# Kernel tuning notes

Hardware: AMD Instinct MI355X
Metric: run time of the kernel (lower is better)

## Reference

```python
import jax, jax.numpy as jnp
import numpy as np

HIDDEN = 512
EMBED = 50
VOCAB = 83


def setup_inputs() -> dict:
    key = jax.random.key(0)
    ks = jax.random.split(key, 20)
    T, B = 600, 256
    s = lambda n: 1.0 / np.sqrt(n)
    inp = {
        "in_char": jax.random.normal(ks[0], (B, VOCAB), jnp.float32),
        "hidden": jax.random.normal(ks[1], (1, B, HIDDEN), jnp.float32),
        "encoder_output": jax.random.normal(ks[2], (T, B, HIDDEN), jnp.float32),
        # attention params
        "W_hp": jax.random.uniform(ks[3], (HIDDEN, HIDDEN), jnp.float32, -s(HIDDEN), s(HIDDEN)),
        "b_hp": jnp.zeros((HIDDEN,), jnp.float32),
        "W_ep": jax.random.uniform(ks[4], (HIDDEN, HIDDEN), jnp.float32, -s(HIDDEN), s(HIDDEN)),
        "b_ep": jnp.zeros((HIDDEN,), jnp.float32),
        "w_v": jax.random.uniform(ks[5], (HIDDEN, 1), jnp.float32, -s(HIDDEN), s(HIDDEN)),
        "b_v": jnp.zeros((1,), jnp.float32),
        # context shrink
        "W_cs": jax.random.uniform(ks[6], (HIDDEN, EMBED * 5), jnp.float32, -s(HIDDEN), s(HIDDEN)),
        "b_cs": jnp.zeros((EMBED * 5,), jnp.float32),
        # embedding
        "emb": jax.random.normal(ks[7], (VOCAB, EMBED), jnp.float32),
        # GRU: input size = 6*EMBED = 300, hidden = 512; gates [r,z,n]
        "W_ih": jax.random.uniform(ks[8], (6 * EMBED, 3 * HIDDEN), jnp.float32, -s(HIDDEN), s(HIDDEN)),
        "b_ih": jnp.zeros((3 * HIDDEN,), jnp.float32),
        "W_hh": jax.random.uniform(ks[9], (HIDDEN, 3 * HIDDEN), jnp.float32, -s(HIDDEN), s(HIDDEN)),
        "b_hh": jnp.zeros((3 * HIDDEN,), jnp.float32),
        # classifier
        "W_out": jax.random.uniform(ks[10], (HIDDEN, VOCAB), jnp.float32, -s(HIDDEN), s(HIDDEN)),
        "b_out": jnp.zeros((VOCAB,), jnp.float32),
    }
    return inp


def reference(in_char, hidden, encoder_output, W_hp, b_hp, W_ep, b_ep, w_v, b_v,
              W_cs, b_cs, emb, W_ih, b_ih, W_hh, b_hh, W_out, b_out):
    # encoder_output: [T, B, H]; hidden: [1, B, H]
    enc_bt = jnp.transpose(encoder_output, (1, 0, 2))  # [B, T, H]
    # Bahdanau additive attention score
    hidden_attn = hidden @ W_hp + b_hp            # [1, B, H]
    hidden_attn = jnp.transpose(hidden_attn, (1, 0, 2))  # [B, 1, H]
    enc_attn = enc_bt @ W_ep + b_ep               # [B, T, H]
    res = jnp.tanh(enc_attn + hidden_attn)        # [B, T, H]
    scores = (res @ w_v + b_v)[..., 0]            # [B, T]
    attn_weights = jax.nn.softmax(scores, axis=1)  # [B, T]
    # context = enc^T @ attn: [B, H]
    context = jnp.einsum('bth,bt->bh', enc_bt, attn_weights)
    context = context @ W_cs + b_cs               # [B, 5*EMBED]
    # embedding of argmax char
    top1 = jnp.argmax(in_char, axis=1)            # [B]
    embed_char = emb[top1]                        # [B, EMBED]
    in_dec = jnp.concatenate([embed_char, context], axis=1)  # [B, 6*EMBED]
    # single GRU step (PyTorch gate order: r, z, n)
    h = hidden[0]                                 # [B, H]
    gi = in_dec @ W_ih + b_ih                     # [B, 3H]
    gh = h @ W_hh + b_hh                          # [B, 3H]
    H = h.shape[1]
    i_r, i_z, i_n = gi[:, :H], gi[:, H:2 * H], gi[:, 2 * H:]
    h_r, h_z, h_n = gh[:, :H], gh[:, H:2 * H], gh[:, 2 * H:]
    r = jax.nn.sigmoid(i_r + h_r)
    z = jax.nn.sigmoid(i_z + h_z)
    n = jnp.tanh(i_n + r * h_n)
    new_h = (1.0 - z) * n + z * h                 # [B, H]
    output = jax.nn.softmax(new_h @ W_out + b_out, axis=1)  # [B, VOCAB]
    return output, new_h[None], attn_weights
```

## Files before the change

### kernel.cpp

```cpp
#include <hip/hip_runtime.h>

typedef unsigned short u16;
typedef unsigned int   u32;
typedef __attribute__((ext_vector_type(8))) short s8v;
typedef __attribute__((ext_vector_type(4))) float f4v;

#define OUT1_OFF 21248
#define OUT2_OFF 152320

__device__ __forceinline__ float b2f(u16 u) { return __uint_as_float(((u32)u) << 16); }
__device__ __forceinline__ u16 f2b(float f) {
  u32 x = __float_as_uint(f);
  x += 0x7fffu + ((x >> 16) & 1u);
  return (u16)(x >> 16);
}
__device__ __forceinline__ float ldf(const void* p, int i, int f32) {
  return f32 ? ((const float*)p)[i] : b2f(((const u16*)p)[i]);
}
__device__ __forceinline__ void stf(void* p, int i, float v, int f32) {
  if (f32) ((float*)p)[i] = v;
  else     ((u16*)p)[i] = f2b(v);
}
__device__ __forceinline__ float tanh_fast(float x) {
  float e = __expf(2.f * x);
  return 1.f - 2.f * __builtin_amdgcn_rcpf(e + 1.f);
}
__device__ __forceinline__ float sigmoid_fast(float x) {
  return __builtin_amdgcn_rcpf(1.f + __expf(-x));
}

__global__ __launch_bounds__(64) void k_detect(const u32* __restrict__ hid, int* __restrict__ flag) {
  int lane = threadIdx.x;
  int cnt = 0;
#pragma unroll
  for (int i = 0; i < 8; i++) {
    u32 w = hid[lane * 8 + i];
    u32 e = (w >> 7) & 0xFF;
    cnt += (e >= 100 && e <= 135) ? 1 : 0;
  }
#pragma unroll
  for (int o = 32; o > 0; o >>= 1) cnt += __shfl_xor(cnt, o);
  if (lane == 0) *flag = (cnt < 400) ? 1 : 0;
}

__global__ __launch_bounds__(256) void k_transpose(const void* __restrict__ in, u16* __restrict__ out,
                                                   const int* __restrict__ flagp) {
  const int f32 = *flagp;
  __shared__ u16 tile[32][33];
  const int bx = blockIdx.x * 32;
  const int by = blockIdx.y * 32;
  const int tx = threadIdx.x, ty = threadIdx.y;
#pragma unroll
  for (int i = 0; i < 4; i++)
    tile[ty + i * 8][tx] = f2b(ldf(in, (by + ty + i * 8) * 512 + bx + tx, f32));
  __syncthreads();
#pragma unroll
  for (int i = 0; i < 4; i++)
    out[(bx + ty + i * 8) * 512 + by + tx] = tile[tx][ty + i * 8];
}

__global__ __launch_bounds__(256) void k_hidden_attn(const void* __restrict__ hidden,
                                                     const void* __restrict__ W_hp,
                                                     const void* __restrict__ b_hp,
                                                     const void* __restrict__ b_ep,
                                                     float* __restrict__ ha2,
                                                     const int* __restrict__ flagp) {
  const int f32 = *flagp;
  const int b0 = blockIdx.x * 8, tid = threadIdx.x;
  __shared__ __align__(16) float hh[512 * 8];
  for (int idx = tid; idx < 4096; idx += 256) {
    int k = idx >> 3, j = idx & 7;
    hh[idx] = ldf(hidden, (b0 + j) * 512 + k, f32);
  }
  __syncthreads();
  const int n0 = tid, n1 = tid + 256;
  float acc0[8], acc1[8];
#pragma unroll
  for (int j = 0; j < 8; j++) { acc0[j] = 0.f; acc1[j] = 0.f; }
  for (int k = 0; k < 512; k++) {
    float w0 = ldf(W_hp, k * 512 + n0, f32);
    float w1 = ldf(W_hp, k * 512 + n1, f32);
    const f4v* hp = (const f4v*)&hh[k * 8];
    f4v ha = hp[0], hb = hp[1];
#pragma unroll
    for (int j = 0; j < 4; j++) {
      acc0[j] += ha[j] * w0; acc1[j] += ha[j] * w1;
      acc0[j + 4] += hb[j] * w0; acc1[j + 4] += hb[j] * w1;
    }
  }
  const float bb0 = ldf(b_hp, n0, f32) + ldf(b_ep, n0, f32);
  const float bb1 = ldf(b_hp, n1, f32) + ldf(b_ep, n1, f32);
#pragma unroll
  for (int j = 0; j < 8; j++) {
    ha2[(b0 + j) * 512 + n0] = acc0[j] + bb0;
    ha2[(b0 + j) * 512 + n1] = acc1[j] + bb1;
  }
}

__global__ __launch_bounds__(256) void k_scores(const void* __restrict__ enc,
                                                const u16* __restrict__ Wt,
                                                const float* __restrict__ ha2,
                                                const void* __restrict__ w_v,
                                                float* __restrict__ partial,
                                                const int* __restrict__ flagp) {
  const int f32 = *flagp;
  __shared__ __align__(16) short As[128 * 64];
  __shared__ __align__(16) short Bs[128 * 64];
  const int tid = threadIdx.x;
  const int ntile = blockIdx.x;
  const int mtile = blockIdx.y;
  const int lane = tid & 63, wave = tid >> 6;
  const int wm = wave >> 1, wn = wave & 1;
  const int lane15 = lane & 15, quad = lane >> 4;

  const u16*   Ab = (const u16*)enc + (size_t)mtile * 128 * 512;
  const float* Af = (const float*)enc + (size_t)mtile * 128 * 512;
  const u16*   Bbase = Wt + (size_t)ntile * 128 * 512;

  int srow[4], sslot[4], skc[4];
#pragma unroll
  for (int c = 0; c < 4; c++) {
    int chunk = c * 256 + tid;
    srow[c] = chunk >> 3;
    sslot[c] = chunk & 7;
    skc[c] = sslot[c] ^ (srow[c] & 7);
  }

  int arow[4], brow[4];
#pragma unroll
  for (int i = 0; i < 4; i++) {
    arow[i] = wm * 64 + i * 16 + lane15;
    brow[i] = wn * 64 + i * 16 + lane15;
  }

  f4v acc[4][4];
#pragma unroll
  for (int i = 0; i < 4; i++)
#pragma unroll
    for (int j = 0; j < 4; j++) acc[i][j] = (f4v){0.f, 0.f, 0.f, 0.f};

  for (int k0 = 0; k0 < 512; k0 += 64) {
    s8v ga[4], gb[4];
    if (f32) {
#pragma unroll
      for (int c = 0; c < 4; c++) {
        const float* s = Af + k0 + srow[c] * 512 + skc[c] * 8;
        f4v lo = *(const f4v*)s, hi = *(const f4v*)(s + 4);
        s8v t;
#pragma unroll
        for (int j = 0; j < 4; j++) { t[j] = (short)f2b(lo[j]); t[j + 4] = (short)f2b(hi[j]); }
        ga[c] = t;
      }
    } else {
#pragma unroll
      for (int c = 0; c < 4; c++) ga[c] = *(const s8v*)(Ab + k0 + srow[c] * 512 + skc[c] * 8);
    }
#pragma unroll
    for (int c = 0; c < 4; c++) gb[c] = *(const s8v*)(Bbase + k0 + srow[c] * 512 + skc[c] * 8);
#pragma unroll
    for (int c = 0; c < 4; c++) *(s8v*)&As[srow[c] * 64 + sslot[c] * 8] = ga[c];
#pragma unroll
    for (int c = 0; c < 4; c++) *(s8v*)&Bs[srow[c] * 64 + sslot[c] * 8] = gb[c];
    __syncthreads();
#pragma unroll
    for (int kk2 = 0; kk2 < 2; kk2++) {
      s8v av[4], bv[4];
#pragma unroll
      for (int i = 0; i < 4; i++) {
        int r = arow[i];
        int kc = (kk2 * 4 + quad) ^ (r & 7);
        av[i] = *(const s8v*)&As[r * 64 + kc * 8];
      }
#pragma unroll
      for (int j = 0; j < 4; j++) {
        int r = brow[j];
        int kc = (kk2 * 4 + quad) ^ (r & 7);
        bv[j] = *(const s8v*)&Bs[r * 64 + kc * 8];
      }
#pragma unroll
      for (int i = 0; i < 4; i++)
#pragma unroll
        for (int j = 0; j < 4; j++)
          acc[i][j] = __builtin_amdgcn_mfma_f32_16x16x32_bf16(av[i], bv[j], acc[i][j], 0, 0, 0);
    }
    __syncthreads();
  }

  float wv[4]; int ng[4];
#pragma unroll
  for (int j = 0; j < 4; j++) {
    ng[j] = ntile * 128 + wn * 64 + j * 16 + lane15;
    wv[j] = ldf(w_v, ng[j], f32);
  }
#pragma unroll
  for (int i = 0; i < 4; i++) {
#pragma unroll
    for (int r = 0; r < 4; r++) {
      int mg = mtile * 128 + wm * 64 + i * 16 + quad * 4 + r;
      int bb = mg & 255, tt = mg >> 8;
      const float* hrow = ha2 + bb * 512;
      float s = 0.f;
#pragma unroll
      for (int j = 0; j < 4; j++)
        s += tanh_fast(acc[i][j][r] + hrow[ng[j]]) * wv[j];
      s += __shfl_xor(s, 1); s += __shfl_xor(s, 2);
      s += __shfl_xor(s, 4); s += __shfl_xor(s, 8);
      if (lane15 == 0) partial[(bb * 600 + tt) * 8 + ntile * 2 + wn] = s;
    }
  }
}

__global__ __launch_bounds__(256) void k_softmax(const float* __restrict__ partial,
                                                 float* __restrict__ attn,
                                                 void* __restrict__ dout,
                                                 const int* __restrict__ flagp) {
  const int f32 = *flagp;
  const int b = blockIdx.x, tid = threadIdx.x;
  float sv[3];
  float m = -1e30f;
#pragma unroll
  for (int ii = 0; ii < 3; ii++) {
    int t = tid + ii * 256;
    float s = -1e30f;
    if (t < 600) {
      const float* p = partial + (size_t)(b * 600 + t) * 8;
      s = ((p[0] + p[1]) + (p[2] + p[3])) + ((p[4] + p[5]) + (p[6] + p[7]));
    }
    sv[ii] = s;
    m = fmaxf(m, s);
  }
#pragma unroll
  for (int o = 32; o > 0; o >>= 1) m = fmaxf(m, __shfl_xor(m, o));
  __shared__ float red[4], redsum[4];
  if ((tid & 63) == 0) red[tid >> 6] = m;
  __syncthreads();
  m = fmaxf(fmaxf(red[0], red[1]), fmaxf(red[2], red[3]));
  float lsum = 0.f, ev[3];
#pragma unroll
  for (int ii = 0; ii < 3; ii++) {
    int t = tid + ii * 256;
    float e = (t < 600) ? __expf(sv[ii] - m) : 0.f;
    ev[ii] = e;
    lsum += e;
  }
#pragma unroll
  for (int o = 32; o > 0; o >>= 1) lsum += __shfl_xor(lsum, o);
  if ((tid & 63) == 0) redsum[tid >> 6] = lsum;
  __syncthreads();
  float inv = 1.f / (redsum[0] + redsum[1] + redsum[2] + redsum[3]);
#pragma unroll
  for (int ii = 0; ii < 3; ii++) {
    int t = tid + ii * 256;
    if (t < 600) {
      float a = ev[ii] * inv;
      attn[b * 600 + t] = a;
      stf(dout, OUT2_OFF + b * 600 + t, a, f32);
    }
  }
}

__global__ __launch_bounds__(256) void k_context(const void* __restrict__ enc,
                                                 const float* __restrict__ attn,
                                                 float* __restrict__ part,
                                                 const int* __restrict__ flagp) {
  const int f32 = *flagp;
  const int b = blockIdx.x, ch = blockIdx.y, tid = threadIdx.x;
  float ax = 0.f, ay = 0.f;
  const int t0 = ch * 75;
  if (f32) {
    const float* ef = (const float*)enc;
    for (int t = t0; t < t0 + 75; t++) {
      float w = attn[b * 600 + t];
      float2 pv = *(const float2*)&ef[((size_t)(t * 256 + b)) * 512 + tid * 2];
      ax += w * pv.x;
      ay += w * pv.y;
    }
  } else {
    const u16* eb = (const u16*)enc;
    for (int t = t0; t < t0 + 75; t++) {
      float w = attn[b * 600 + t];
      u32 pv = *(const u32*)&eb[((size_t)(t * 256 + b)) * 512 + tid * 2];
      ax += w * b2f((u16)(pv & 0xffff));
      ay += w * b2f((u16)(pv >> 16));
    }
  }
  float2 o; o.x = ax; o.y = ay;
  *(float2*)&part[((size_t)(ch * 256 + b)) * 512 + tid * 2] = o;
}

__global__ __launch_bounds__(256) void k_decode_pre(const void* __restrict__ in_char,
                                                    const float* __restrict__ part,
                                                    const void* __restrict__ W_cs,
                                                    const void* __restrict__ b_cs,
                                                    const void* __restrict__ emb,
                                                    float* __restrict__ indec,
                                                    const int* __restrict__ flagp) {
  const int f32 = *flagp;
  const int b = blockIdx.x, tid = threadIdx.x;
  __shared__ float ctx[512];
  __shared__ int topi;
  for (int h = tid; h < 512; h += 256) {
    float s = 0.f;
#pragma unroll
    for (int c = 0; c < 8; c++) s += part[((size_t)(c * 256 + b)) * 512 + h];
    ctx[h] = s;
  }
  if (tid == 0) {
    float best = -1e30f; int bi = 0;
    for (int i = 0; i < 83; i++) {
      float v = ldf(in_char, b * 83 + i, f32);
      if (v > best) { best = v; bi = i; }
    }
    topi = bi;
  }
  __syncthreads();
  if (tid < 50) indec[b * 300 + tid] = ldf(emb, topi * 50 + tid, f32);
  if (tid < 250) {
    float acc = ldf(b_cs, tid, f32);
    for (int k = 0; k < 512; k++) acc += ctx[k] * ldf(W_cs, k * 250 + tid, f32);
    indec[b * 300 + 50 + tid] = acc;
  }
}

__global__ __launch_bounds__(256) void k_gates(const float* __restrict__ indec,
                                               const void* __restrict__ hidden,
                                               const void* __restrict__ W_ih,
                                               const void* __restrict__ b_ih,
                                               const void* __restrict__ W_hh,
                                               const void* __restrict__ b_hh,
                                               float* __restrict__ gi,
                                               float* __restrict__ gh,
                                               const int* __restrict__ flagp) {
  const int f32 = *flagp;
  const int tid = threadIdx.x;
  const int n = blockIdx.x * 256 + tid;
  const int b0 = blockIdx.y * 8;
  const int z = blockIdx.z;
  __shared__ __align__(16) float src[512 * 8];
  if (z) {
    for (int idx = tid; idx < 4096; idx += 256) {
      int k = idx >> 3, j = idx & 7;
      src[idx] = ldf(hidden, (b0 + j) * 512 + k, f32);
    }
  } else {
    for (int idx = tid; idx < 2400; idx += 256) {
      int k = idx >> 3, j = idx & 7;
      src[idx] = indec[(b0 + j) * 300 + k];
    }
  }
  __syncthreads();
  const int K = z ? 512 : 300;
  const void* W = z ? W_hh : W_ih;
  const float bias = ldf(z ? b_hh : b_ih, n, f32);
  float acc[8];
#pragma unroll
  for (int j = 0; j < 8; j++) acc[j] = bias;
  for (int k = 0; k < K; k++) {
    float w = ldf(W, k * 1536 + n, f32);
    const f4v* hp = (const f4v*)&src[k * 8];
    f4v h0 = hp[0], h1 = hp[1];
#pragma unroll
    for (int j = 0; j < 4; j++) {
      acc[j] += h0[j] * w;
      acc[j + 4] += h1[j] * w;
    }
  }
  float* dst = z ? gh : gi;
#pragma unroll
  for (int j = 0; j < 8; j++) dst[(b0 + j) * 1536 + n] = acc[j];
}

__global__ __launch_bounds__(512) void k_gru(const float* __restrict__ gi,
                                             const float* __restrict__ gh,
                                             const void* __restrict__ hidden,
                                             float* __restrict__ newh,
                                             void* __restrict__ dout,
                                             const int* __restrict__ flagp) {
  const int f32 = *flagp;
  const int b = blockIdx.x, n = threadIdx.x;
  const float* gib = gi + b * 1536;
  const float* ghb = gh + b * 1536;
  float r = sigmoid_fast(gib[n] + ghb[n]);
  float z = sigmoid_fast(gib[512 + n] + ghb[512 + n]);
  float nn = tanh_fast(gib[1024 + n] + r * ghb[1024 + n]);
  float h = ldf(hidden, b * 512 + n, f32);
  float v = (1.f - z) * nn + z * h;
  newh[b * 512 + n] = v;
  stf(dout, OUT1_OFF + b * 512 + n, v, f32);
}

__global__ __launch_bounds__(128) void k_out_softmax(const float* __restrict__ newh,
                                                     const void* __restrict__ W_out,
                                                     const void* __restrict__ b_out,
                                                     void* __restrict__ dout,
                                                     const int* __restrict__ flagp) {
  const int f32 = *flagp;
  const int b = blockIdx.x, tid = threadIdx.x;
  __shared__ float h[512];
  __shared__ float lg[83];
  __shared__ float mx, sm;
  for (int i = tid; i < 512; i += 128) h[i] = newh[b * 512 + i];
  __syncthreads();
  float acc = 0.f;
  if (tid < 83) {
    acc = ldf(b_out, tid, f32);
    for (int k = 0; k < 512; k++) acc += h[k] * ldf(W_out, k * 83 + tid, f32);
    lg[tid] = acc;
  }
  __syncthreads();
  if (tid == 0) {
    float m = -1e30f;
    for (int i = 0; i < 83; i++) m = fmaxf(m, lg[i]);
    mx = m;
  }
  __syncthreads();
  float e = 0.f;
  if (tid < 83) { e = __expf(acc - mx); lg[tid] = e; }
  __syncthreads();
  if (tid == 0) {
    float s = 0.f;
    for (int i = 0; i < 83; i++) s += lg[i];
    sm = s;
  }
  __syncthreads();
  if (tid < 83) stf(dout, b * 83 + tid, e / sm, f32);
}

extern "C" void kernel_launch(void* const* d_in, const int* in_sizes, int n_in,
                              void* d_out, int out_size, void* d_ws, size_t ws_size,
                              hipStream_t stream) {
  const void* in_char = d_in[0];
  const void* hidden  = d_in[1];
  const void* enc     = d_in[2];
  const void* W_hp    = d_in[3];
  const void* b_hp    = d_in[4];
  const void* W_ep    = d_in[5];
  const void* b_ep    = d_in[6];
  const void* w_v     = d_in[7];
  const void* W_cs    = d_in[9];
  const void* b_cs    = d_in[10];
  const void* emb     = d_in[11];
  const void* W_ih    = d_in[12];
  const void* b_ih    = d_in[13];
  const void* W_hh    = d_in[14];
  const void* b_hh    = d_in[15];
  const void* W_out   = d_in[16];
  const void* b_out   = d_in[17];

  char* ws = (char*)d_ws;
  int*   flag  = (int*)(ws);
  u16*   Wt    = (u16*)(ws + 256);
  float* ha2   = (float*)(ws + 524544);
  float* attn  = (float*)(ws + 1048832);
  float* indec = (float*)(ws + 1663232);
  float* newh  = (float*)(ws + 1970432);
  char*  big   = ws + 2494720;
  float* part8 = (float*)big;
  float* ctxp  = (float*)big;
  float* gi    = (float*)big;
  float* gh    = (float*)(big + 1572864);

  k_detect<<<1, 64, 0, stream>>>((const u32*)hidden, flag);
  k_transpose<<<dim3(16, 16), dim3(32, 8), 0, stream>>>(W_ep, Wt, flag);
  k_hidden_attn<<<32, 256, 0, stream>>>(hidden, W_hp, b_hp, b_ep, ha2, flag);
  k_scores<<<dim3(4, 1200), 256, 0, stream>>>(enc, Wt, ha2, w_v, part8, flag);
  k_softmax<<<256, 256, 0, stream>>>(part8, attn, d_out, flag);
  k_context<<<dim3(256, 8), 256, 0, stream>>>(enc, attn, ctxp, flag);
  k_decode_pre<<<256, 256, 0, stream>>>(in_char, ctxp, W_cs, b_cs, emb, indec, flag);
  k_gates<<<dim3(6, 32, 2), 256, 0, stream>>>(indec, hidden, W_ih, b_ih, W_hh, b_hh, gi, gh, flag);
  k_gru<<<256, 512, 0, stream>>>(gi, gh, hidden, newh, d_out, flag);
  k_out_softmax<<<256, 128, 0, stream>>>(newh, W_out, b_out, d_out, flag);
}
```

Measured before the change: 1.065 ms.

## Pre-convert encoder to bf16 once and stream it via direct-to-LDS loads

Removes the runtime dtype-detection kernel and flag, hardcoding fp32 inputs. When the workspace is large enough, a prep kernel converts the whole encoder tensor to bf16 once. The score GEMM then loads tiles with global_load_lds directly into shared memory, and the context reduction reads the half-size bf16 copy. The score grid is also remapped to a 1-D grid with a grouped mtile/ntile order for cache locality. The extra conversion pass costs a full fp32 read plus a bf16 write of the encoder, in exchange for cheaper reads in the two later kernels.

```diff
diff --git a/kernel.cpp b/kernel.cpp
--- a/kernel.cpp
+++ b/kernel.cpp
@@ -14,13 +14,6 @@
   x += 0x7fffu + ((x >> 16) & 1u);
   return (u16)(x >> 16);
 }
-__device__ __forceinline__ float ldf(const void* p, int i, int f32) {
-  return f32 ? ((const float*)p)[i] : b2f(((const u16*)p)[i]);
-}
-__device__ __forceinline__ void stf(void* p, int i, float v, int f32) {
-  if (f32) ((float*)p)[i] = v;
-  else     ((u16*)p)[i] = f2b(v);
-}
 __device__ __forceinline__ float tanh_fast(float x) {
   float e = __expf(2.f * x);
   return 1.f - 2.f * __builtin_amdgcn_rcpf(e + 1.f);
@@ -28,49 +21,44 @@
 __device__ __forceinline__ float sigmoid_fast(float x) {
   return __builtin_amdgcn_rcpf(1.f + __expf(-x));
 }
-
-__global__ __launch_bounds__(64) void k_detect(const u32* __restrict__ hid, int* __restrict__ flag) {
-  int lane = threadIdx.x;
-  int cnt = 0;
-#pragma unroll
-  for (int i = 0; i < 8; i++) {
-    u32 w = hid[lane * 8 + i];
-    u32 e = (w >> 7) & 0xFF;
-    cnt += (e >= 100 && e <= 135) ? 1 : 0;
-  }
-#pragma unroll
-  for (int o = 32; o > 0; o >>= 1) cnt += __shfl_xor(cnt, o);
-  if (lane == 0) *flag = (cnt < 400) ? 1 : 0;
-}
-
-__global__ __launch_bounds__(256) void k_transpose(const void* __restrict__ in, u16* __restrict__ out,
-                                                   const int* __restrict__ flagp) {
-  const int f32 = *flagp;
+__device__ __forceinline__ void gl16(const void* g, void* l) {
+  __builtin_amdgcn_global_load_lds((const __attribute__((address_space(1))) u32*)g,
+                                   (__attribute__((address_space(3))) u32*)l, 16, 0, 0);
+}
+
+__global__ __launch_bounds__(256) void k_prep(const f4v* __restrict__ in, s8v* __restrict__ out) {
+  int i = blockIdx.x * 256 + threadIdx.x;
+  f4v a = in[2 * i], b = in[2 * i + 1];
+  s8v t;
+#pragma unroll
+  for (int j = 0; j < 4; j++) { t[j] = (short)f2b(a[j]); t[4 + j] = (short)f2b(b[j]); }
+  out[i] = t;
+}
+
+__global__ __launch_bounds__(256) void k_transpose(const float* __restrict__ in, u16* __restrict__ out) {
   __shared__ u16 tile[32][33];
   const int bx = blockIdx.x * 32;
   const int by = blockIdx.y * 32;
   const int tx = threadIdx.x, ty = threadIdx.y;
 #pragma unroll
   for (int i = 0; i < 4; i++)
-    tile[ty + i * 8][tx] = f2b(ldf(in, (by + ty + i * 8) * 512 + bx + tx, f32));
+    tile[ty + i * 8][tx] = f2b(in[(by + ty + i * 8) * 512 + bx + tx]);
   __syncthreads();
 #pragma unroll
   for (int i = 0; i < 4; i++)
     out[(bx + ty + i * 8) * 512 + by + tx] = tile[tx][ty + i * 8];
 }
 
-__global__ __launch_bounds__(256) void k_hidden_attn(const void* __restrict__ hidden,
-                                                     const void* __restrict__ W_hp,
-                                                     const void* __restrict__ b_hp,
-                                                     const void* __restrict__ b_ep,
-                                                     float* __restrict__ ha2,
-                                                     const int* __restrict__ flagp) {
-  const int f32 = *flagp;
+__global__ __launch_bounds__(256) void k_hidden_attn(const float* __restrict__ hidden,
+                                                     const float* __restrict__ W_hp,
+                                                     const float* __restrict__ b_hp,
+                                                     const float* __restrict__ b_ep,
+                                                     float* __restrict__ ha2) {
   const int b0 = blockIdx.x * 8, tid = threadIdx.x;
   __shared__ __align__(16) float hh[512 * 8];
   for (int idx = tid; idx < 4096; idx += 256) {
     int k = idx >> 3, j = idx & 7;
-    hh[idx] = ldf(hidden, (b0 + j) * 512 + k, f32);
+    hh[idx] = hidden[(b0 + j) * 512 + k];
   }
   __syncthreads();
   const int n0 = tid, n1 = tid + 256;
@@ -78,8 +66,8 @@
 #pragma unroll
   for (int j = 0; j < 8; j++) { acc0[j] = 0.f; acc1[j] = 0.f; }
   for (int k = 0; k < 512; k++) {
-    float w0 = ldf(W_hp, k * 512 + n0, f32);
-    float w1 = ldf(W_hp, k * 512 + n1, f32);
+    float w0 = W_hp[k * 512 + n0];
+    float w1 = W_hp[k * 512 + n1];
     const f4v* hp = (const f4v*)&hh[k * 8];
     f4v ha = hp[0], hb = hp[1];
 #pragma unroll
@@ -88,8 +76,8 @@
       acc0[j + 4] += hb[j] * w0; acc1[j + 4] += hb[j] * w1;
     }
   }
-  const float bb0 = ldf(b_hp, n0, f32) + ldf(b_ep, n0, f32);
-  const float bb1 = ldf(b_hp, n1, f32) + ldf(b_ep, n1, f32);
+  const float bb0 = b_hp[n0] + b_ep[n0];
+  const float bb1 = b_hp[n1] + b_ep[n1];
 #pragma unroll
   for (int j = 0; j < 8; j++) {
     ha2[(b0 + j) * 512 + n0] = acc0[j] + bb0;
@@ -97,24 +85,121 @@
   }
 }
 
-__global__ __launch_bounds__(256) void k_scores(const void* __restrict__ enc,
-                                                const u16* __restrict__ Wt,
-                                                const float* __restrict__ ha2,
-                                                const void* __restrict__ w_v,
-                                                float* __restrict__ partial,
-                                                const int* __restrict__ flagp) {
-  const int f32 = *flagp;
+__global__ __launch_bounds__(256) void k_scores_bf(const u16* __restrict__ encb,
+                                                   const u16* __restrict__ Wt,
+                                                   const float* __restrict__ ha2,
+                                                   const float* __restrict__ w_v,
+                                                   float* __restrict__ partial) {
   __shared__ __align__(16) short As[128 * 64];
   __shared__ __align__(16) short Bs[128 * 64];
   const int tid = threadIdx.x;
-  const int ntile = blockIdx.x;
-  const int mtile = blockIdx.y;
+  const int id = blockIdx.x;
+  const int x = id & 7, jj = id >> 3;
+  const int mtile = x * 150 + (jj >> 2);
+  const int ntile = jj & 3;
   const int lane = tid & 63, wave = tid >> 6;
   const int wm = wave >> 1, wn = wave & 1;
   const int lane15 = lane & 15, quad = lane >> 4;
 
-  const u16*   Ab = (const u16*)enc + (size_t)mtile * 128 * 512;
-  const float* Af = (const float*)enc + (size_t)mtile * 128 * 512;
+  const u16* Abase = encb + (size_t)mtile * 128 * 512;
+  const u16* Bbase = Wt + (size_t)ntile * 128 * 512;
+
+  int srow[4], skc[4];
+#pragma unroll
+  for (int c = 0; c < 4; c++) {
+    int chunk = c * 256 + tid;
+    srow[c] = chunk >> 3;
+    skc[c] = (chunk & 7) ^ (srow[c] & 7);
+  }
+
+  int arow[4], brow[4];
+#pragma unroll
+  for (int i = 0; i < 4; i++) {
+    arow[i] = wm * 64 + i * 16 + lane15;
+    brow[i] = wn * 64 + i * 16 + lane15;
+  }
+
+  f4v acc[4][4];
+#pragma unroll
+  for (int i = 0; i < 4; i++)
+#pragma unroll
+    for (int j = 0; j < 4; j++) acc[i][j] = (f4v){0.f, 0.f, 0.f, 0.f};
+
+  for (int k0 = 0; k0 < 512; k0 += 64) {
+    const u16* Ak = Abase + k0;
+    const u16* Bk = Bbase + k0;
+#pragma unroll
+    for (int c = 0; c < 4; c++)
+      gl16(Ak + srow[c] * 512 + skc[c] * 8, (char*)As + c * 4096 + tid * 16);
+#pragma unroll
+    for (int c = 0; c < 4; c++)
+      gl16(Bk + srow[c] * 512 + skc[c] * 8, (char*)Bs + c * 4096 + tid * 16);
+    __syncthreads();
+#pragma unroll
+    for (int kk2 = 0; kk2 < 2; kk2++) {
+      s8v av[4], bv[4];
+#pragma unroll
+      for (int i = 0; i < 4; i++) {
+        int r = arow[i];
+        int kc = (kk2 * 4 + quad) ^ (r & 7);
+        av[i] = *(const s8v*)&As[r * 64 + kc * 8];
+      }
+#pragma unroll
+      for (int j = 0; j < 4; j++) {
+        int r = brow[j];
+        int kc = (kk2 * 4 + quad) ^ (r & 7);
+        bv[j] = *(const s8v*)&Bs[r * 64 + kc * 8];
+      }
+#pragma unroll
+      for (int i = 0; i < 4; i++)
+#pragma unroll
+        for (int j = 0; j < 4; j++)
+          acc[i][j] = __builtin_amdgcn_mfma_f32_16x16x32_bf16(av[i], bv[j], acc[i][j], 0, 0, 0);
+    }
+    __syncthreads();
+  }
+
+  float wv[4]; int ng[4];
+#pragma unroll
+  for (int j = 0; j < 4; j++) {
+    ng[j] = ntile * 128 + wn * 64 + j * 16 + lane15;
+    wv[j] = w_v[ng[j]];
+  }
+#pragma unroll
+  for (int i = 0; i < 4; i++) {
+#pragma unroll
+    for (int r = 0; r < 4; r++) {
+      int mg = mtile * 128 + wm * 64 + i * 16 + quad * 4 + r;
+      int bb = mg & 255, tt = mg >> 8;
+      const float* hrow = ha2 + bb * 512;
+      float s = 0.f;
+#pragma unroll
+      for (int j = 0; j < 4; j++)
+        s += tanh_fast(acc[i][j][r] + hrow[ng[j]]) * wv[j];
+      s += __shfl_xor(s, 1); s += __shfl_xor(s, 2);
+      s += __shfl_xor(s, 4); s += __shfl_xor(s, 8);
+      if (lane15 == 0) partial[(bb * 600 + tt) * 8 + ntile * 2 + wn] = s;
+    }
+  }
+}
+
+__global__ __launch_bounds__(256) void k_scores_f32(const float* __restrict__ enc,
+                                                    const u16* __restrict__ Wt,
+                                                    const float* __restrict__ ha2,
+                                                    const float* __restrict__ w_v,
+                                                    float* __restrict__ partial) {
+  __shared__ __align__(16) short As[128 * 64];
+  __shared__ __align__(16) short Bs[128 * 64];
+  const int tid = threadIdx.x;
+  const int id = blockIdx.x;
+  const int x = id & 7, jj = id >> 3;
+  const int mtile = x * 150 + (jj >> 2);
+  const int ntile = jj & 3;
+  const int lane = tid & 63, wave = tid >> 6;
+  const int wm = wave >> 1, wn = wave & 1;
+  const int lane15 = lane & 15, quad = lane >> 4;
+
+  const float* Af = enc + (size_t)mtile * 128 * 512;
   const u16*   Bbase = Wt + (size_t)ntile * 128 * 512;
 
   int srow[4], sslot[4], skc[4];
@@ -125,14 +210,12 @@
     sslot[c] = chunk & 7;
     skc[c] = sslot[c] ^ (srow[c] & 7);
   }
-
   int arow[4], brow[4];
 #pragma unroll
   for (int i = 0; i < 4; i++) {
     arow[i] = wm * 64 + i * 16 + lane15;
     brow[i] = wn * 64 + i * 16 + lane15;
   }
-
   f4v acc[4][4];
 #pragma unroll
   for (int i = 0; i < 4; i++)
@@ -141,19 +224,14 @@
 
   for (int k0 = 0; k0 < 512; k0 += 64) {
     s8v ga[4], gb[4];
-    if (f32) {
-#pragma unroll
-      for (int c = 0; c < 4; c++) {
-        const float* s = Af + k0 + srow[c] * 512 + skc[c] * 8;
-        f4v lo = *(const f4v*)s, hi = *(const f4v*)(s + 4);
-        s8v t;
-#pragma unroll
-        for (int j = 0; j < 4; j++) { t[j] = (short)f2b(lo[j]); t[j + 4] = (short)f2b(hi[j]); }
-        ga[c] = t;
-      }
-    } else {
-#pragma unroll
-      for (int c = 0; c < 4; c++) ga[c] = *(const s8v*)(Ab + k0 + srow[c] * 512 + skc[c] * 8);
+#pragma unroll
+    for (int c = 0; c < 4; c++) {
+      const float* s = Af + k0 + srow[c] * 512 + skc[c] * 8;
+      f4v lo = *(const f4v*)s, hi = *(const f4v*)(s + 4);
+      s8v t;
+#pragma unroll
+      for (int j = 0; j < 4; j++) { t[j] = (short)f2b(lo[j]); t[j + 4] = (short)f2b(hi[j]); }
+      ga[c] = t;
     }
 #pragma unroll
     for (int c = 0; c < 4; c++) gb[c] = *(const s8v*)(Bbase + k0 + srow[c] * 512 + skc[c] * 8);
@@ -190,7 +268,7 @@
 #pragma unroll
   for (int j = 0; j < 4; j++) {
     ng[j] = ntile * 128 + wn * 64 + j * 16 + lane15;
-    wv[j] = ldf(w_v, ng[j], f32);
+    wv[j] = w_v[ng[j]];
   }
 #pragma unroll
   for (int i = 0; i < 4; i++) {
@@ -212,9 +290,7 @@
 
 __global__ __launch_bounds__(256) void k_softmax(const float* __restrict__ partial,
                                                  float* __restrict__ attn,
-                                                 void* __restrict__ dout,
-                                                 const int* __restrict__ flagp) {
-  const int f32 = *flagp;
+                                                 float* __restrict__ out2) {
   const int b = blockIdx.x, tid = threadIdx.x;
   float sv[3];
   float m = -1e30f;
@@ -254,48 +330,49 @@
     if (t < 600) {
       float a = ev[ii] * inv;
       attn[b * 600 + t] = a;
-      stf(dout, OUT2_OFF + b * 600 + t, a, f32);
-    }
-  }
-}
-
-__global__ __launch_bounds__(256) void k_context(const void* __restrict__ enc,
-                                                 const float* __restrict__ attn,
-                                                 float* __restrict__ part,
-                                                 const int* __restrict__ flagp) {
-  const int f32 = *flagp;
+      out2[b * 600 + t] = a;
+    }
+  }
+}
+
+__global__ __launch_bounds__(256) void k_context_bf(const u16* __restrict__ encb,
+                                                    const float* __restrict__ attn,
+                                                    float* __restrict__ part) {
   const int b = blockIdx.x, ch = blockIdx.y, tid = threadIdx.x;
   float ax = 0.f, ay = 0.f;
   const int t0 = ch * 75;
-  if (f32) {
-    const float* ef = (const float*)enc;
-    for (int t = t0; t < t0 + 75; t++) {
-      float w = attn[b * 600 + t];
-      float2 pv = *(const float2*)&ef[((size_t)(t * 256 + b)) * 512 + tid * 2];
-      ax += w * pv.x;
-      ay += w * pv.y;
-    }
-  } else {
-    const u16* eb = (const u16*)enc;
-    for (int t = t0; t < t0 + 75; t++) {
-      float w = attn[b * 600 + t];
-      u32 pv = *(const u32*)&eb[((size_t)(t * 256 + b)) * 512 + tid * 2];
-      ax += w * b2f((u16)(pv & 0xffff));
-      ay += w * b2f((u16)(pv >> 16));
-    }
+  for (int t = t0; t < t0 + 75; t++) {
+    float w = attn[b * 600 + t];
+    u32 pv = *(const u32*)&encb[((size_t)(t * 256 + b)) * 512 + tid * 2];
+    ax += w * b2f((u16)(pv & 0xffff));
+    ay += w * b2f((u16)(pv >> 16));
   }
   float2 o; o.x = ax; o.y = ay;
   *(float2*)&part[((size_t)(ch * 256 + b)) * 512 + tid * 2] = o;
 }
 
-__global__ __launch_bounds__(256) void k_decode_pre(const void* __restrict__ in_char,
+__global__ __launch_bounds__(256) void k_context_f32(const float* __restrict__ enc,
+                                                     const float* __restrict__ attn,
+                                                     float* __restrict__ part) {
+  const int b = blockIdx.x, ch = blockIdx.y, tid = threadIdx.x;
+  float ax = 0.f, ay = 0.f;
+  const int t0 = ch * 75;
+  for (int t = t0; t < t0 + 75; t++) {
+    float w = attn[b * 600 + t];
+    float2 pv = *(const float2*)&enc[((size_t)(t * 256 + b)) * 512 + tid * 2];
+    ax += w * pv.x;
+    ay += w * pv.y;
+  }
+  float2 o; o.x = ax; o.y = ay;
+  *(float2*)&part[((size_t)(ch * 256 + b)) * 512 + tid * 2] = o;
+}
+
+__global__ __launch_bounds__(256) void k_decode_pre(const float* __restrict__ in_char,
                                                     const float* __restrict__ part,
-                                                    const void* __restrict__ W_cs,
-                                                    const void* __restrict__ b_cs,
-                                                    const void* __restrict__ emb,
-                                                    float* __restrict__ indec,
-                                                    const int* __restrict__ flagp) {
-  const int f32 = *flagp;
+                                                    const float* __restrict__ W_cs,
+                                                    const float* __restrict__ b_cs,
+                                                    const float* __restrict__ emb,
+                                                    float* __restrict__ indec) {
   const int b = blockIdx.x, tid = threadIdx.x;
   __shared__ float ctx[512];
   __shared__ int topi;
@@ -308,30 +385,28 @@
   if (tid == 0) {
     float best = -1e30f; int bi = 0;
     for (int i = 0; i < 83; i++) {
-      float v = ldf(in_char, b * 83 + i, f32);
+      float v = in_char[b * 83 + i];
       if (v > best) { best = v; bi = i; }
     }
     topi = bi;
   }
   __syncthreads();
-  if (tid < 50) indec[b * 300 + tid] = ldf(emb, topi * 50 + tid, f32);
+  if (tid < 50) indec[b * 300 + tid] = emb[topi * 50 + tid];
   if (tid < 250) {
-    float acc = ldf(b_cs, tid, f32);
-    for (int k = 0; k < 512; k++) acc += ctx[k] * ldf(W_cs, k * 250 + tid, f32);
+    float acc = b_cs[tid];
+    for (int k = 0; k < 512; k++) acc += ctx[k] * W_cs[k * 250 + tid];
     indec[b * 300 + 50 + tid] = acc;
   }
 }
 
 __global__ __launch_bounds__(256) void k_gates(const float* __restrict__ indec,
-                                               const void* __restrict__ hidden,
-                                               const void* __restrict__ W_ih,
-                                               const void* __restrict__ b_ih,
-                                               const void* __restrict__ W_hh,
-                                               const void* __restrict__ b_hh,
+                                               const float* __restrict__ hidden,
+                                               const float* __restrict__ W_ih,
+                                               const float* __restrict__ b_ih,
+                                               const float* __restrict__ W_hh,
+                                               const float* __restrict__ b_hh,
                                                float* __restrict__ gi,
-                                               float* __restrict__ gh,
-                                               const int* __restrict__ flagp) {
-  const int f32 = *flagp;
+                                               float* __restrict__ gh) {
   const int tid = threadIdx.x;
   const int n = blockIdx.x * 256 + tid;
   const int b0 = blockIdx.y * 8;
@@ -340,7 +415,7 @@
   if (z) {
     for (int idx = tid; idx < 4096; idx += 256) {
       int k = idx >> 3, j = idx & 7;
-      src[idx] = ldf(hidden, (b0 + j) * 512 + k, f32);
+      src[idx] = hidden[(b0 + j) * 512 + k];
     }
   } else {
     for (int idx = tid; idx < 2400; idx += 256) {
@@ -350,13 +425,13 @@
   }
   __syncthreads();
   const int K = z ? 512 : 300;
-  const void* W = z ? W_hh : W_ih;
-  const float bias = ldf(z ? b_hh : b_ih, n, f32);
+  const float* W = (z ? W_hh : W_ih) + n;
+  const float bias = (z ? b_hh : b_ih)[n];
   float acc[8];
 #pragma unroll
   for (int j = 0; j < 8; j++) acc[j] = bias;
   for (int k = 0; k < K; k++) {
-    float w = ldf(W, k * 1536 + n, f32);
+    float w = W[k * 1536];
     const f4v* hp = (const f4v*)&src[k * 8];
     f4v h0 = hp[0], h1 = hp[1];
 #pragma unroll
@@ -372,29 +447,25 @@
 
 __global__ __launch_bounds__(512) void k_gru(const float* __restrict__ gi,
                                              const float* __restrict__ gh,
-                                             const void* __restrict__ hidden,
+                                             const float* __restrict__ hidden,
                                              float* __restrict__ newh,
-                                             void* __restrict__ dout,
-                                             const int* __restrict__ flagp) {
-  const int f32 = *flagp;
+                                             float* __restrict__ out1) {
   const int b = blockIdx.x, n = threadIdx.x;
   const float* gib = gi + b * 1536;
   const float* ghb = gh + b * 1536;
   float r = sigmoid_fast(gib[n] + ghb[n]);
   float z = sigmoid_fast(gib[512 + n] + ghb[512 + n]);
   float nn = tanh_fast(gib[1024 + n] + r * ghb[1024 + n]);
-  float h = ldf(hidden, b * 512 + n, f32);
+  float h = hidden[b * 512 + n];
   float v = (1.f - z) * nn + z * h;
   newh[b * 512 + n] = v;
-  stf(dout, OUT1_OFF + b * 512 + n, v, f32);
+  out1[b * 512 + n] = v;
 }
 
 __global__ __launch_bounds__(128) void k_out_softmax(const float* __restrict__ newh,
-                                                     const void* __restrict__ W_out,
-                                                     const void* __restrict__ b_out,
-                                                     void* __restrict__ dout,
-                                                     const int* __restrict__ flagp) {
-  const int f32 = *flagp;
+                                                     const float* __restrict__ W_out,
+                                                     const float* __restrict__ b_out,
+                                                     float* __restrict__ out0) {
   const int b = blockIdx.x, tid = threadIdx.x;
   __shared__ float h[512];
   __shared__ float lg[83];
@@ -403,8 +474,8 @@
   __syncthreads();
   float acc = 0.f;
   if (tid < 83) {
-    acc = ldf(b_out, tid, f32);
-    for (int k = 0; k < 512; k++) acc += h[k] * ldf(W_out, k * 83 + tid, f32);
+    acc = b_out[tid];
+    for (int k = 0; k < 512; k++) acc += h[k] * W_out[k * 83 + tid];
     lg[tid] = acc;
   }
   __syncthreads();
@@ -423,51 +494,63 @@
     sm = s;
   }
   __syncthreads();
-  if (tid < 83) stf(dout, b * 83 + tid, e / sm, f32);
+  if (tid < 83) out0[b * 83 + tid] = e / sm;
 }
 
 extern "C" void kernel_launch(void* const* d_in, const int* in_sizes, int n_in,
                               void* d_out, int out_size, void* d_ws, size_t ws_size,
                               hipStream_t stream) {
-  const void* in_char = d_in[0];
-  const void* hidden  = d_in[1];
-  const void* enc     = d_in[2];
-  const void* W_hp    = d_in[3];
-  const void* b_hp    = d_in[4];
-  const void* W_ep    = d_in[5];
-  const void* b_ep    = d_in[6];
-  const void* w_v     = d_in[7];
-  const void* W_cs    = d_in[9];
-  const void* b_cs    = d_in[10];
-  const void* emb     = d_in[11];
-  const void* W_ih    = d_in[12];
-  const void* b_ih    = d_in[13];
-  const void* W_hh    = d_in[14];
-  const void* b_hh    = d_in[15];
-  const void* W_out   = d_in[16];
-  const void* b_out   = d_in[17];
+  const float* in_char = (const float*)d_in[0];
+  const float* hidden  = (const float*)d_in[1];
+  const float* enc     = (const float*)d_in[2];
+  const float* W_hp    = (const float*)d_in[3];
+  const float* b_hp    = (const float*)d_in[4];
+  const float* W_ep    = (const float*)d_in[5];
+  const float* b_ep    = (const float*)d_in[6];
+  const float* w_v     = (const float*)d_in[7];
+  const float* W_cs    = (const float*)d_in[9];
+  const float* b_cs    = (const float*)d_in[10];
+  const float* emb     = (const float*)d_in[11];
+  const float* W_ih    = (const float*)d_in[12];
+  const float* b_ih    = (const float*)d_in[13];
+  const float* W_hh    = (const float*)d_in[14];
+  const float* b_hh    = (const float*)d_in[15];
+  const float* W_out   = (const float*)d_in[16];
+  const float* b_out   = (const float*)d_in[17];
 
   char* ws = (char*)d_ws;
-  int*   flag  = (int*)(ws);
-  u16*   Wt    = (u16*)(ws + 256);
-  float* ha2   = (float*)(ws + 524544);
-  float* attn  = (float*)(ws + 1048832);
-  float* indec = (float*)(ws + 1663232);
-  float* newh  = (float*)(ws + 1970432);
-  char*  big   = ws + 2494720;
+  u16*   Wt    = (u16*)(ws);
+  float* ha2   = (float*)(ws + 524288);
+  float* attn  = (float*)(ws + 1048576);
+  float* indec = (float*)(ws + 1662976);
+  float* newh  = (float*)(ws + 1970176);
+  char*  big   = ws + 2494464;
   float* part8 = (float*)big;
   float* ctxp  = (float*)big;
   float* gi    = (float*)big;
   float* gh    = (float*)(big + 1572864);
-
-  k_detect<<<1, 64, 0, stream>>>((const u32*)hidden, flag);
-  k_transpose<<<dim3(16, 16), dim3(32, 8), 0, stream>>>(W_ep, Wt, flag);
-  k_hidden_attn<<<32, 256, 0, stream>>>(hidden, W_hp, b_hp, b_ep, ha2, flag);
-  k_scores<<<dim3(4, 1200), 256, 0, stream>>>(enc, Wt, ha2, w_v, part8, flag);
-  k_softmax<<<256, 256, 0, stream>>>(part8, attn, d_out, flag);
-  k_context<<<dim3(256, 8), 256, 0, stream>>>(enc, attn, ctxp, flag);
-  k_decode_pre<<<256, 256, 0, stream>>>(in_char, ctxp, W_cs, b_cs, emb, indec, flag);
-  k_gates<<<dim3(6, 32, 2), 256, 0, stream>>>(indec, hidden, W_ih, b_ih, W_hh, b_hh, gi, gh, flag);
-  k_gru<<<256, 512, 0, stream>>>(gi, gh, hidden, newh, d_out, flag);
-  k_out_softmax<<<256, 128, 0, stream>>>(newh, W_out, b_out, d_out, flag);
-}
+  u16*   encb  = (u16*)(ws + 8388608);
+  const bool big_ws = ws_size >= (size_t)(8388608 + 157286400);
+
+  float* out0 = (float*)d_out;
+  float* out1 = out0 + OUT1_OFF;
+  float* out2 = out0 + OUT2_OFF;
+
+  if (big_ws)
+    k_prep<<<38400, 256, 0, stream>>>((const f4v*)enc, (s8v*)encb);
+  k_transpose<<<dim3(16, 16), dim3(32, 8), 0, stream>>>(W_ep, Wt);
+  k_hidden_attn<<<32, 256, 0, stream>>>(hidden, W_hp, b_hp, b_ep, ha2);
+  if (big_ws)
+    k_scores_bf<<<4800, 256, 0, stream>>>(encb, Wt, ha2, w_v, part8);
+  else
+    k_scores_f32<<<4800, 256, 0, stream>>>(enc, Wt, ha2, w_v, part8);
+  k_softmax<<<256, 256, 0, stream>>>(part8, attn, out2);
+  if (big_ws)
+    k_context_bf<<<dim3(256, 8), 256, 0, stream>>>(encb, attn, ctxp);
+  else
+    k_context_f32<<<dim3(256, 8), 256, 0, stream>>>(enc, attn, ctxp);
+  k_decode_pre<<<256, 256, 0, stream>>>(in_char, ctxp, W_cs, b_cs, emb, indec);
+  k_gates<<<dim3(6, 32, 2), 256, 0, stream>>>(indec, hidden, W_ih, b_ih, W_hh, b_hh, gi, gh);
+  k_gru<<<256, 512, 0, stream>>>(gi, gh, hidden, newh, out1);
+  k_out_softmax<<<256, 128, 0, stream>>>(newh, W_out, b_out, out0);
+}
```

Result: faster. 865.1 us (-18.8%).
